# Optimization experiments

Hardware: AMD Instinct MI355X
Metric: run time of the kernel (lower is better)

## Reference

```python
import jax, jax.numpy as jnp
import numpy as np

RADIUS = 0.1
K = 32
NUM_GROUPS = 8
EPS = 1e-5
B, N = 2, 4096
IN_DIM = 13
OUT_DIMS = (64, 64, 128)


def _safe_norm(x, axis=-1, keepdims=False):
    # 2-norm with zero (not NaN) gradient at 0; forward identical to jnp.linalg.norm
    sq = jnp.sum(x * x, axis=axis, keepdims=keepdims)
    nz = sq > 0
    return jnp.where(nz, jnp.sqrt(jnp.where(nz, sq, 1.0)), 0.0)


def _angle(v1, v2):
    y = _safe_norm(jnp.cross(v1, v2), axis=-1)
    x = jnp.sum(v1 * v2, axis=-1)
    deg = (y == 0) & (x == 0)  # degenerate pairs (e.g. self-neighbor): atan2(0,0)=0
    return jnp.where(deg, 0.0, jnp.arctan2(y, jnp.where(deg, 1.0, x)))


def _ball_group(xyz, radius, k):
    # xyz: (B,N,3) -> neighbor indices (B,N,K); pad out-of-radius slots with first valid idx
    b, n, _ = xyz.shape
    sq = jnp.sum((xyz[:, :, None, :] - xyz[:, None, :, :]) ** 2, axis=-1)  # (B,N,N)
    idx = jnp.broadcast_to(jnp.arange(n, dtype=jnp.int32), (b, n, n))
    idx = jnp.where(sq > radius * radius, n, idx)
    idx = jnp.sort(idx, axis=-1)[:, :, :k]  # (B,N,K)
    first = idx[:, :, :1]
    return jnp.where(idx == n, first, idx)


def _group_norm(x, gamma, beta):
    # x: (B,C,K,N), torch GroupNorm(8, C) semantics (biased var, eps=1e-5)
    b, c, k, n = x.shape
    xg = x.reshape(b, NUM_GROUPS, c // NUM_GROUPS, k, n)
    m = jnp.mean(xg, axis=(2, 3, 4), keepdims=True)
    v = jnp.var(xg, axis=(2, 3, 4), keepdims=True)
    xn = ((xg - m) * jax.lax.rsqrt(v + EPS)).reshape(b, c, k, n)
    return xn * gamma[None, :, None, None] + beta[None, :, None, None]


def _forward(feature, xyz, conv0_w, gn0_g, gn0_b, conv1_w, gn1_g, gn1_b,
             conv2_w, gn2_g, gn2_b, wa, wb, wc):
    b = xyz.shape[0]
    idx = _ball_group(xyz, RADIUS, K)                     # (B,N,K) int32
    bidx = jnp.arange(b)[:, None, None]
    grouped_xyz = xyz[bidx, idx]                          # (B,N,K,3)
    grouped_xyz1 = grouped_xyz - xyz[:, :, None, :]       # relative coords
    dists = _safe_norm(grouped_xyz1, axis=-1, keepdims=True)
    grouped_n = feature[bidx, idx]                        # grouped normals (B,N,K,3)
    new_points = jnp.concatenate([grouped_xyz1, dists, grouped_n], axis=-1)  # (B,N,K,7)

    nr = feature[:, :, None, :]                           # (B,N,1,3)
    ppf = jnp.stack([_angle(nr, grouped_xyz1),
                     _angle(grouped_n, grouped_xyz1),
                     _angle(nr, grouped_n)], axis=-1)     # (B,N,K,3)

    xyz6 = jnp.concatenate([jnp.broadcast_to(xyz[:, :, None, :], grouped_xyz.shape),
                            grouped_xyz], axis=-1)        # (B,N,K,6)
    fused = jnp.concatenate([wa * xyz6, wb * new_points[..., :4], wc * ppf], axis=-1)  # (B,N,K,13)

    x = jnp.transpose(fused, (0, 3, 2, 1))                # (B,13,K,N)
    layers = [(conv0_w, gn0_g, gn0_b), (conv1_w, gn1_g, gn1_b), (conv2_w, gn2_g, gn2_b)]
    for i, (w, g, bb) in enumerate(layers):
        x = jnp.einsum('oc,bckn->bokn', w, x)             # 1x1 conv, no bias
        x = _group_norm(x, g, bb)
        if i != len(layers) - 1:
            x = jax.nn.relu(x)
    out = jnp.max(jax.nn.relu(x), axis=2)                 # (B,128,N)
    x = jnp.max(x, axis=2)                                # (B,128,N)
    return (out, x)


def setup_inputs() -> dict:
    key = jax.random.key(0)
    ks = jax.random.split(key, 8)
    xyz = jax.random.uniform(ks[0], (B, N, 3), dtype=jnp.float32)
    feature = jax.random.normal(ks[1], (B, N, 3), dtype=jnp.float32)
    feature = feature / _safe_norm(feature, axis=-1, keepdims=True)  # unit normals
    inp = {'feature': feature, 'xyz': xyz}
    dims = [IN_DIM] + list(OUT_DIMS)
    for i in range(3):
        scale = 1.0 / np.sqrt(dims[i])
        inp[f'conv{i}_w'] = (jax.random.normal(ks[2 + i], (dims[i + 1], dims[i]), dtype=jnp.float32) * scale)
        inp[f'gn{i}_g'] = jnp.ones((dims[i + 1],), jnp.float32)
        inp[f'gn{i}_b'] = jnp.zeros((dims[i + 1],), jnp.float32)
    inp['wa'] = jnp.ones((1,), jnp.float32)
    inp['wb'] = jnp.ones((1,), jnp.float32)
    inp['wc'] = jnp.ones((1,), jnp.float32)
    return inp


def reference(feature, xyz, conv0_w, gn0_g, gn0_b, conv1_w, gn1_g, gn1_b,
              conv2_w, gn2_g, gn2_b, wa, wb, wc):
    return _forward(feature, xyz, conv0_w, gn0_g, gn0_b, conv1_w, gn1_g, gn1_b,
                    conv2_w, gn2_g, gn2_b, wa, wb, wc)
```

## Files before the change

kernel.cpp:

```cpp
#include <hip/hip_runtime.h>
#include <hip/hip_bf16.h>

#define DEVINL __device__ __forceinline__

typedef short short8 __attribute__((ext_vector_type(8)));
typedef float f32x4 __attribute__((ext_vector_type(4)));

namespace {
constexpr int NB = 2;
constexpr int NN = 4096;
constexpr int KK = 32;
constexpr int NP = NN * KK;
constexpr float R2 = 0.01f;
constexpr float GEPS = 1e-5f;
}

DEVINL ushort2 splitbf(float v) {
    unsigned int b = __float_as_uint(v);
    unsigned int hb = b & 0xffff0000u;
    float r = v - __uint_as_float(hb);
    unsigned int lb = __float_as_uint(r);
    ushort2 res;
    res.x = (unsigned short)(hb >> 16);
    res.y = (unsigned short)(lb >> 16);
    return res;
}

DEVINL float angle3(float ax, float ay, float az, float bx, float by, float bz) {
    float crx = ay * bz - az * by;
    float cry = az * bx - ax * bz;
    float crz = ax * by - ay * bx;
    float sq = crx * crx + cry * cry + crz * crz;
    float yv = sq > 0.f ? sqrtf(sq) : 0.f;
    float xv = ax * bx + ay * by + az * bz;
    if (yv == 0.f && xv == 0.f) return 0.f;
    return atan2f(yv, xv);
}

template <int NV>
DEVINL float blockReducePart(float* vals) {
    #pragma unroll
    for (int m = 1; m < 64; m <<= 1) {
        #pragma unroll
        for (int q = 0; q < NV; ++q) vals[q] += __shfl_xor(vals[q], m, 64);
    }
    __shared__ float red[4][NV];
    int lane = threadIdx.x & 63, w = threadIdx.x >> 6;
    if (lane == 0) {
        #pragma unroll
        for (int q = 0; q < NV; ++q) red[w][q] = vals[q];
    }
    __syncthreads();
    float v = 0.f;
    if ((int)threadIdx.x < NV)
        v = red[0][threadIdx.x] + red[1][threadIdx.x] +
            red[2][threadIdx.x] + red[3][threadIdx.x];
    return v;
}

__global__ __launch_bounds__(256) void k_red(const float* __restrict__ part,
                                             float* __restrict__ stats, int nblk) {
    int o = blockIdx.x;
    const float* p = part + (size_t)o * nblk;
    float s = 0.f;
    for (int i = threadIdx.x; i < nblk; i += 256) s += p[i];
    #pragma unroll
    for (int m = 1; m < 64; m <<= 1) s += __shfl_xor(s, m, 64);
    __shared__ float r[4];
    if ((threadIdx.x & 63) == 0) r[threadIdx.x >> 6] = s;
    __syncthreads();
    if (threadIdx.x == 0) stats[o] = r[0] + r[1] + r[2] + r[3];
}

__global__ void k_prep(const float* __restrict__ w0, const float* __restrict__ w1,
                       const float* __restrict__ w2, float* __restrict__ w0t,
                       short* __restrict__ a1hi, short* __restrict__ a1lo,
                       short* __restrict__ a2hi, short* __restrict__ a2lo) {
    int t = threadIdx.x;
    for (int x = t; x < 64 * 13; x += 256) { int o = x / 13, c = x % 13; w0t[c * 64 + o] = w0[x]; }
    for (int x = t; x < 512; x += 256) {
        int lane = x & 63, ks = (x >> 6) & 1, mt = x >> 7;
        int o = mt * 16 + (lane & 15);
        int cb = ks * 32 + (lane >> 4) * 8;
        #pragma unroll
        for (int e = 0; e < 8; ++e) {
            ushort2 s = splitbf(w1[o * 64 + cb + e]);
            a1hi[x * 8 + e] = (short)s.x;
            a1lo[x * 8 + e] = (short)s.y;
        }
    }
    for (int x = t; x < 1024; x += 256) {
        int lane = x & 63, ks = (x >> 6) & 1, mt = x >> 7;
        int o = mt * 16 + (lane & 15);
        int cb = ks * 32 + (lane >> 4) * 8;
        #pragma unroll
        for (int e = 0; e < 8; ++e) {
            ushort2 s = splitbf(w2[o * 64 + cb + e]);
            a2hi[x * 8 + e] = (short)s.x;
            a2lo[x * 8 + e] = (short)s.y;
        }
    }
}

__global__ __launch_bounds__(256) void k_ball(const float* __restrict__ xyz,
                                              int* __restrict__ idx) {
    int wid = blockIdx.x * 4 + (threadIdx.x >> 6);
    int lane = threadIdx.x & 63;
    int b = wid >> 12;
    int i = wid & (NN - 1);
    const float* xb = xyz + b * NN * 3;
    float cx = xb[i * 3 + 0], cy = xb[i * 3 + 1], cz = xb[i * 3 + 2];
    int* out = idx + wid * KK;
    int cnt = 0;
    int firstj = 0;
    for (int base = 0; base < NN; base += 64) {
        int j = base + lane;
        float dx = xb[j * 3 + 0] - cx;
        float dy = xb[j * 3 + 1] - cy;
        float dz = xb[j * 3 + 2] - cz;
        float d2 = __fadd_rn(__fadd_rn(__fmul_rn(dx, dx), __fmul_rn(dy, dy)), __fmul_rn(dz, dz));
        bool valid = d2 <= R2;
        unsigned long long m = __ballot(valid);
        if (cnt == 0 && m != 0ull) firstj = base + (int)__builtin_ctzll(m);
        int pos = (int)__popcll(m & ((1ull << lane) - 1ull));
        if (valid && (cnt + pos) < KK) out[cnt + pos] = j;
        cnt += (int)__popcll(m);
        if (cnt >= KK) break;
    }
    if (cnt < KK) {
        int kpad = cnt + lane;
        if (kpad < KK) out[kpad] = firstj;
    }
}

__global__ __launch_bounds__(256) void k_feat(
    const float* __restrict__ xyz, const float* __restrict__ feat,
    const int* __restrict__ idx, const float* __restrict__ w0t,
    const float* __restrict__ wap, const float* __restrict__ wbp,
    const float* __restrict__ wcp, float* __restrict__ f13,
    float* __restrict__ part0) {
    int t = blockIdx.x * 256 + threadIdx.x;
    int b = t / NP, r = t % NP;
    int i = r >> 5;
    int j = idx[t];
    const float* xb = xyz + b * NN * 3;
    const float* fb = feat + b * NN * 3;
    float cx = xb[i * 3], cy = xb[i * 3 + 1], cz = xb[i * 3 + 2];
    float nx = fb[i * 3], ny = fb[i * 3 + 1], nz = fb[i * 3 + 2];
    float gx = xb[j * 3], gy = xb[j * 3 + 1], gz = xb[j * 3 + 2];
    float mx = fb[j * 3], my = fb[j * 3 + 1], mz = fb[j * 3 + 2];
    float dx = gx - cx, dy = gy - cy, dz = gz - cz;
    float d2 = dx * dx + dy * dy + dz * dz;
    float dist = d2 > 0.f ? sqrtf(d2) : 0.f;
    float a1 = angle3(nx, ny, nz, dx, dy, dz);
    float a2 = angle3(mx, my, mz, dx, dy, dz);
    float a3 = angle3(nx, ny, nz, mx, my, mz);
    float WA = wap[0], WB = wbp[0], WC = wcp[0];
    float f[13] = {WA * cx, WA * cy, WA * cz, WA * gx, WA * gy, WA * gz,
                   WB * dx, WB * dy, WB * dz, WB * dist, WC * a1, WC * a2, WC * a3};
    float* fo = f13 + (size_t)b * 13 * NP + r;
    #pragma unroll
    for (int c = 0; c < 13; ++c) fo[(size_t)c * NP] = f[c];
    float acc[64];
    #pragma unroll
    for (int o = 0; o < 64; ++o) acc[o] = 0.f;
    #pragma unroll
    for (int c = 0; c < 13; ++c) {
        float v = f[c];
        const float* wr = w0t + c * 64;
        #pragma unroll
        for (int o = 0; o < 64; ++o) acc[o] = fmaf(wr[o], v, acc[o]);
    }
    float vals[16];
    #pragma unroll
    for (int g = 0; g < 8; ++g) {
        float sv = 0.f, sq = 0.f;
        #pragma unroll
        for (int c2 = 0; c2 < 8; ++c2) { float v = acc[g * 8 + c2]; sv += v; sq = fmaf(v, v, sq); }
        vals[g * 2] = sv; vals[g * 2 + 1] = sq;
    }
    float pv = blockReducePart<16>(vals);
    if ((int)threadIdx.x < 16) {
        int blkInB = blockIdx.x & 511;
        part0[(size_t)(b * 16 + threadIdx.x) * 512 + blkInB] = pv;
    }
}

__global__ __launch_bounds__(256) void k_conv01m(
    const float* __restrict__ f13, const float* __restrict__ stats0,
    const float* __restrict__ g0, const float* __restrict__ b0,
    const float* __restrict__ w0t,
    const short* __restrict__ a1hi, const short* __restrict__ a1lo,
    float* __restrict__ y1, float* __restrict__ part1) {
    __shared__ __align__(16) short Xhi[128 * 64];
    __shared__ __align__(16) short Xlo[128 * 64];
    __shared__ float Aff[128];
    int t = threadIdx.x, blk = blockIdx.x;
    int b = blk >> 10;
    int blkInB = blk & 1023;
    int pbase = blkInB << 7;
    if (t < 64) {
        int c = t, g = c >> 3;
        const float inv = 1.f / 1048576.f;
        float s = stats0[b * 16 + g * 2], q = stats0[b * 16 + g * 2 + 1];
        float mean = s * inv;
        float var = q * inv - mean * mean;
        float rstd = rsqrtf(var + GEPS);
        float a = rstd * g0[c];
        Aff[c] = a; Aff[64 + c] = fmaf(-mean, a, b0[c]);
    }
    __syncthreads();
    {
        int p = t & 127, chalf = t >> 7;
        const float* fi = f13 + (size_t)b * 13 * NP + pbase + p;
        float fv[13];
        #pragma unroll
        for (int c = 0; c < 13; ++c) fv[c] = fi[(size_t)c * NP];
        float acc[32];
        #pragma unroll
        for (int o = 0; o < 32; ++o) acc[o] = 0.f;
        #pragma unroll
        for (int c = 0; c < 13; ++c) {
            const float* wr = w0t + c * 64 + chalf * 32;
            #pragma unroll
            for (int o = 0; o < 32; ++o) acc[o] = fmaf(wr[o], fv[c], acc[o]);
        }
        int swz = (p & 7) << 4;
        #pragma unroll
        for (int jc = 0; jc < 4; ++jc) {
            int hw[4], lw[4];
            #pragma unroll
            for (int u = 0; u < 4; ++u) {
                int o0 = jc * 8 + u * 2;
                int ch0 = chalf * 32 + o0;
                float v0 = fmaxf(fmaf(Aff[ch0], acc[o0], Aff[64 + ch0]), 0.f);
                float v1 = fmaxf(fmaf(Aff[ch0 + 1], acc[o0 + 1], Aff[64 + ch0 + 1]), 0.f);
                ushort2 s0 = splitbf(v0), s1 = splitbf(v1);
                hw[u] = (int)((unsigned)s0.x | ((unsigned)s1.x << 16));
                lw[u] = (int)((unsigned)s0.y | ((unsigned)s1.y << 16));
            }
            int off = p * 128 + ((chalf * 64 + jc * 16) ^ swz);
            *reinterpret_cast<int4*>((char*)Xhi + off) = make_int4(hw[0], hw[1], hw[2], hw[3]);
            *reinterpret_cast<int4*>((char*)Xlo + off) = make_int4(lw[0], lw[1], lw[2], lw[3]);
        }
    }
    __syncthreads();
    {
        int w = t >> 6, lane = t & 63, col = lane & 15, kb = lane >> 4;
        short8 whi[2], wlo[2];
        #pragma unroll
        for (int ks = 0; ks < 2; ++ks) {
            int fi_ = ((w * 2 + ks) * 64 + lane) * 8;
            whi[ks] = *reinterpret_cast<const short8*>(a1hi + fi_);
            wlo[ks] = *reinterpret_cast<const short8*>(a1lo + fi_);
        }
        float sv = 0.f, sq = 0.f;
        int swzr = (col & 7) << 4;
        float* yb = y1 + (size_t)b * 64 * NP + pbase + col;
        #pragma unroll 2
        for (int s = 0; s < 8; ++s) {
            int rowoff = (s * 16 + col) * 128;
            f32x4 d = {0.f, 0.f, 0.f, 0.f};
            #pragma unroll
            for (int ks = 0; ks < 2; ++ks) {
                int boff = rowoff + ((ks * 64 + kb * 16) ^ swzr);
                short8 bh = *reinterpret_cast<const short8*>((char*)Xhi + boff);
                short8 bl = *reinterpret_cast<const short8*>((char*)Xlo + boff);
                d = __builtin_amdgcn_mfma_f32_16x16x32_bf16(whi[ks], bh, d, 0, 0, 0);
                d = __builtin_amdgcn_mfma_f32_16x16x32_bf16(whi[ks], bl, d, 0, 0, 0);
                d = __builtin_amdgcn_mfma_f32_16x16x32_bf16(wlo[ks], bh, d, 0, 0, 0);
            }
            #pragma unroll
            for (int q = 0; q < 4; ++q) {
                int ch = w * 16 + kb * 4 + q;
                yb[(size_t)ch * NP + s * 16] = d[q];
                sv += d[q];
                sq = fmaf(d[q], d[q], sq);
            }
        }
        #pragma unroll
        for (int m = 1; m <= 16; m <<= 1) {
            sv += __shfl_xor(sv, m, 64);
            sq += __shfl_xor(sq, m, 64);
        }
        if ((lane & 31) == 0) {
            int grp = w * 2 + (lane >> 5);
            size_t o = (size_t)(b * 16 + grp * 2) * 1024 + blkInB;
            part1[o] = sv;
            part1[o + 1024] = sq;
        }
    }
}

__global__ __launch_bounds__(256) void k_conv2m(
    const float* __restrict__ y1, const float* __restrict__ stats1,
    const float* __restrict__ g1, const float* __restrict__ b1,
    const float* __restrict__ g2,
    const short* __restrict__ a2hi, const short* __restrict__ a2lo,
    float* __restrict__ ext, float* __restrict__ part2) {
    __shared__ __align__(16) short Xhi[128 * 64];
    __shared__ __align__(16) short Xlo[128 * 64];
    __shared__ float Aff[128];
    int t = threadIdx.x, blk = blockIdx.x;
    int b = blk >> 10;
    int blkInB = blk & 1023;
    int pbase = blkInB << 7;
    if (t < 64) {
        int c = t, g = c >> 3;
        const float inv = 1.f / 1048576.f;
        float s = stats1[b * 16 + g * 2], q = stats1[b * 16 + g * 2 + 1];
        float mean = s * inv;
        float var = q * inv - mean * mean;
        float rstd = rsqrtf(var + GEPS);
        float a = rstd * g1[c];
        Aff[c] = a; Aff[64 + c] = fmaf(-mean, a, b1[c]);
    }
    __syncthreads();
    {
        int p = t & 127, cblk = t >> 7;
        const float* yi = y1 + (size_t)b * 64 * NP + pbase + p;
        int swz = (p & 7) << 4;
        #pragma unroll
        for (int jc = 0; jc < 4; ++jc) {
            int hw[4], lw[4];
            #pragma unroll
            for (int u = 0; u < 4; ++u) {
                int ch0 = cblk * 32 + jc * 8 + u * 2;
                float v0 = yi[(size_t)ch0 * NP];
                float v1 = yi[(size_t)(ch0 + 1) * NP];
                v0 = fmaxf(fmaf(Aff[ch0], v0, Aff[64 + ch0]), 0.f);
                v1 = fmaxf(fmaf(Aff[ch0 + 1], v1, Aff[64 + ch0 + 1]), 0.f);
                ushort2 s0 = splitbf(v0), s1 = splitbf(v1);
                hw[u] = (int)((unsigned)s0.x | ((unsigned)s1.x << 16));
                lw[u] = (int)((unsigned)s0.y | ((unsigned)s1.y << 16));
            }
            int off = p * 128 + ((cblk * 64 + jc * 16) ^ swz);
            *reinterpret_cast<int4*>((char*)Xhi + off) = make_int4(hw[0], hw[1], hw[2], hw[3]);
            *reinterpret_cast<int4*>((char*)Xlo + off) = make_int4(lw[0], lw[1], lw[2], lw[3]);
        }
    }
    __syncthreads();
    {
        int w = t >> 6, lane = t & 63, col = lane & 15, kb = lane >> 4;
        int mt0 = w * 2;
        short8 whi[2][2], wlo[2][2];
        #pragma unroll
        for (int m = 0; m < 2; ++m)
            #pragma unroll
            for (int ks = 0; ks < 2; ++ks) {
                int fi_ = (((mt0 + m) * 2 + ks) * 64 + lane) * 8;
                whi[m][ks] = *reinterpret_cast<const short8*>(a2hi + fi_);
                wlo[m][ks] = *reinterpret_cast<const short8*>(a2lo + fi_);
            }
        float gv[2][4];
        #pragma unroll
        for (int m = 0; m < 2; ++m)
            #pragma unroll
            for (int q = 0; q < 4; ++q) gv[m][q] = g2[(mt0 + m) * 16 + kb * 4 + q];
        float sv[2] = {0.f, 0.f}, sq[2] = {0.f, 0.f};
        int swzr = (col & 7) << 4;
        int ibase = pbase >> 5;
        #pragma unroll
        for (int sp = 0; sp < 4; ++sp) {
            f32x4 dp0[2], dp1[2];
            #pragma unroll
            for (int ss = 0; ss < 2; ++ss) {
                int rowoff = ((sp * 2 + ss) * 16 + col) * 128;
                short8 bh[2], bl[2];
                #pragma unroll
                for (int ks = 0; ks < 2; ++ks) {
                    int boff = rowoff + ((ks * 64 + kb * 16) ^ swzr);
                    bh[ks] = *reinterpret_cast<const short8*>((char*)Xhi + boff);
                    bl[ks] = *reinterpret_cast<const short8*>((char*)Xlo + boff);
                }
                #pragma unroll
                for (int m = 0; m < 2; ++m) {
                    f32x4 d = {0.f, 0.f, 0.f, 0.f};
                    #pragma unroll
                    for (int ks = 0; ks < 2; ++ks) {
                        d = __builtin_amdgcn_mfma_f32_16x16x32_bf16(whi[m][ks], bh[ks], d, 0, 0, 0);
                        d = __builtin_amdgcn_mfma_f32_16x16x32_bf16(whi[m][ks], bl[ks], d, 0, 0, 0);
                        d = __builtin_amdgcn_mfma_f32_16x16x32_bf16(wlo[m][ks], bh[ks], d, 0, 0, 0);
                    }
                    #pragma unroll
                    for (int q = 0; q < 4; ++q) {
                        sv[m] += d[q];
                        sq[m] = fmaf(d[q], d[q], sq[m]);
                    }
                    if (ss == 0) dp0[m] = d; else dp1[m] = d;
                }
            }
            #pragma unroll
            for (int m = 0; m < 2; ++m) {
                float e[4];
                #pragma unroll
                for (int q = 0; q < 4; ++q) {
                    bool mx = gv[m][q] >= 0.f;
                    e[q] = mx ? fmaxf(dp0[m][q], dp1[m][q]) : fminf(dp0[m][q], dp1[m][q]);
                    #pragma unroll
                    for (int sh = 1; sh <= 8; sh <<= 1) {
                        float o = __shfl_xor(e[q], sh, 64);
                        e[q] = mx ? fmaxf(e[q], o) : fminf(e[q], o);
                    }
                }
                if (col == 0) {
                    #pragma unroll
                    for (int q = 0; q < 4; ++q) {
                        int ch = (mt0 + m) * 16 + kb * 4 + q;
                        ext[((size_t)b * 128 + ch) * NN + ibase + sp] = e[q];
                    }
                }
            }
        }
        #pragma unroll
        for (int m = 0; m < 2; ++m) {
            #pragma unroll
            for (int sh = 1; sh <= 32; sh <<= 1) {
                sv[m] += __shfl_xor(sv[m], sh, 64);
                sq[m] += __shfl_xor(sq[m], sh, 64);
            }
        }
        if (lane == 0) {
            #pragma unroll
            for (int m = 0; m < 2; ++m) {
                size_t o = (size_t)(b * 16 + (mt0 + m) * 2) * 1024 + blkInB;
                part2[o] = sv[m];
                part2[o + 1024] = sq[m];
            }
        }
    }
}

__global__ __launch_bounds__(256) void k_final(
    const float* __restrict__ ext, const float* __restrict__ stats2,
    const float* __restrict__ g2, const float* __restrict__ b2,
    float* __restrict__ outp) {
    __shared__ float A[128], Bc[128];
    int t = blockIdx.x * 256 + threadIdx.x;
    int b = t / (128 * NN);
    int rem = t - b * 128 * NN;
    int c = rem >> 12;
    if (threadIdx.x < 128) {
        int cc = threadIdx.x, g = cc >> 4;
        const float inv = 1.f / 2097152.f;
        float s = stats2[b * 16 + g * 2], q = stats2[b * 16 + g * 2 + 1];
        float mean = s * inv;
        float var = q * inv - mean * mean;
        float rstd = rsqrtf(var + GEPS);
        float a = rstd * g2[cc];
        A[cc] = a; Bc[cc] = fmaf(-mean, a, b2[cc]);
    }
    __syncthreads();
    float v = ext[t];
    float val = fmaf(A[c], v, Bc[c]);
    outp[t] = fmaxf(val, 0.f);
    outp[NB * 128 * NN + t] = val;
}

extern "C" void kernel_launch(void* const* d_in, const int* in_sizes, int n_in,
                              void* d_out, int out_size, void* d_ws, size_t ws_size,
                              hipStream_t stream) {
    const float* feat = (const float*)d_in[0];
    const float* xyz  = (const float*)d_in[1];
    const float* w0 = (const float*)d_in[2];
    const float* g0 = (const float*)d_in[3];
    const float* b0 = (const float*)d_in[4];
    const float* w1 = (const float*)d_in[5];
    const float* g1 = (const float*)d_in[6];
    const float* b1 = (const float*)d_in[7];
    const float* w2 = (const float*)d_in[8];
    const float* g2 = (const float*)d_in[9];
    const float* b2 = (const float*)d_in[10];
    const float* wa = (const float*)d_in[11];
    const float* wb = (const float*)d_in[12];
    const float* wc = (const float*)d_in[13];

    char* ws = (char*)d_ws;
    float* stats = (float*)ws;
    float* w0t  = (float*)(ws + 4096);
    short* a1hi = (short*)(ws + 16384);
    short* a1lo = (short*)(ws + 24576);
    short* a2hi = (short*)(ws + 32768);
    short* a2lo = (short*)(ws + 49152);
    int*   idx  = (int*)(ws + 65536);
    float* part0 = (float*)(ws + 1179648);
    float* part1 = (float*)(ws + 1245184);
    float* part2 = (float*)(ws + 1376256);
    float* f13  = (float*)(ws + (2ull << 20));
    float* y1   = (float*)(ws + (16ull << 20));
    float* ext  = (float*)(ws + (80ull << 20));

    hipLaunchKernelGGL(k_prep, dim3(1), dim3(256), 0, stream,
                       w0, w1, w2, w0t, a1hi, a1lo, a2hi, a2lo);
    hipLaunchKernelGGL(k_ball, dim3((NB * NN) / 4), dim3(256), 0, stream, xyz, idx);
    hipLaunchKernelGGL(k_feat, dim3((NB * NP) / 256), dim3(256), 0, stream,
                       xyz, feat, idx, w0t, wa, wb, wc, f13, part0);
    hipLaunchKernelGGL(k_red, dim3(32), dim3(256), 0, stream, part0, stats, 512);
    hipLaunchKernelGGL(k_conv01m, dim3((NB * NP) / 128), dim3(256), 0, stream,
                       f13, stats, g0, b0, w0t, a1hi, a1lo, y1, part1);
    hipLaunchKernelGGL(k_red, dim3(32), dim3(256), 0, stream, part1, stats + 32, 1024);
    hipLaunchKernelGGL(k_conv2m, dim3((NB * NP) / 128), dim3(256), 0, stream,
                       y1, stats + 32, g1, b1, g2, a2hi, a2lo, ext, part2);
    hipLaunchKernelGGL(k_red, dim3(32), dim3(256), 0, stream, part2, stats + 64, 1024);
    hipLaunchKernelGGL(k_final, dim3((NB * 128 * NN) / 256), dim3(256), 0, stream,
                       ext, stats + 64, g2, b2, (float*)d_out);
}
```

Before: 214.9 us.

## Recompute conv0/conv1 inside conv2 kernel instead of storing y1 intermediate

The first conv1 pass now only computes group-norm statistics and no longer writes the 64-channel y1 tensor. The conv2 kernel recomputes conv0, its norm and ReLU, and the conv1 MFMA from f13. It then applies the second norm and ReLU in registers and restages the result in shared memory for conv2. This removes a large global write and read of y1, at the cost of recomputing conv0/conv1, reading f13 twice, and higher register pressure and extra barriers in the fused kernel.

```diff
diff --git a/kernel.cpp b/kernel.cpp
--- a/kernel.cpp
+++ b/kernel.cpp
@@ -186,12 +186,12 @@
     }
 }
 
-__global__ __launch_bounds__(256) void k_conv01m(
+__global__ __launch_bounds__(256) void k_stats01(
     const float* __restrict__ f13, const float* __restrict__ stats0,
     const float* __restrict__ g0, const float* __restrict__ b0,
     const float* __restrict__ w0t,
     const short* __restrict__ a1hi, const short* __restrict__ a1lo,
-    float* __restrict__ y1, float* __restrict__ part1) {
+    float* __restrict__ part1) {
     __shared__ __align__(16) short Xhi[128 * 64];
     __shared__ __align__(16) short Xlo[128 * 64];
     __shared__ float Aff[128];
@@ -256,7 +256,6 @@
         }
         float sv = 0.f, sq = 0.f;
         int swzr = (col & 7) << 4;
-        float* yb = y1 + (size_t)b * 64 * NP + pbase + col;
         #pragma unroll 2
         for (int s = 0; s < 8; ++s) {
             int rowoff = (s * 16 + col) * 128;
@@ -272,8 +271,6 @@
             }
             #pragma unroll
             for (int q = 0; q < 4; ++q) {
-                int ch = w * 16 + kb * 4 + q;
-                yb[(size_t)ch * NP + s * 16] = d[q];
                 sv += d[q];
                 sq = fmaf(d[q], d[q], sq);
             }
@@ -292,15 +289,19 @@
     }
 }
 
-__global__ __launch_bounds__(256) void k_conv2m(
-    const float* __restrict__ y1, const float* __restrict__ stats1,
+__global__ __launch_bounds__(256) void k_fused2(
+    const float* __restrict__ f13, const float* __restrict__ stats0,
+    const float* __restrict__ g0, const float* __restrict__ b0,
+    const float* __restrict__ w0t,
+    const short* __restrict__ a1hi, const short* __restrict__ a1lo,
+    const float* __restrict__ stats1,
     const float* __restrict__ g1, const float* __restrict__ b1,
     const float* __restrict__ g2,
     const short* __restrict__ a2hi, const short* __restrict__ a2lo,
     float* __restrict__ ext, float* __restrict__ part2) {
     __shared__ __align__(16) short Xhi[128 * 64];
     __shared__ __align__(16) short Xlo[128 * 64];
-    __shared__ float Aff[128];
+    __shared__ float Aff[256];
     int t = threadIdx.x, blk = blockIdx.x;
     int b = blk >> 10;
     int blkInB = blk & 1023;
@@ -308,40 +309,110 @@
     if (t < 64) {
         int c = t, g = c >> 3;
         const float inv = 1.f / 1048576.f;
-        float s = stats1[b * 16 + g * 2], q = stats1[b * 16 + g * 2 + 1];
+        float s = stats0[b * 16 + g * 2], q = stats0[b * 16 + g * 2 + 1];
         float mean = s * inv;
         float var = q * inv - mean * mean;
         float rstd = rsqrtf(var + GEPS);
-        float a = rstd * g1[c];
-        Aff[c] = a; Aff[64 + c] = fmaf(-mean, a, b1[c]);
+        float a = rstd * g0[c];
+        Aff[c] = a; Aff[64 + c] = fmaf(-mean, a, b0[c]);
+        float s1 = stats1[b * 16 + g * 2], q1 = stats1[b * 16 + g * 2 + 1];
+        float mean1 = s1 * inv;
+        float var1 = q1 * inv - mean1 * mean1;
+        float rstd1 = rsqrtf(var1 + GEPS);
+        float a1 = rstd1 * g1[c];
+        Aff[128 + c] = a1; Aff[192 + c] = fmaf(-mean1, a1, b1[c]);
     }
     __syncthreads();
     {
-        int p = t & 127, cblk = t >> 7;
-        const float* yi = y1 + (size_t)b * 64 * NP + pbase + p;
+        int p = t & 127, chalf = t >> 7;
+        const float* fi = f13 + (size_t)b * 13 * NP + pbase + p;
+        float fv[13];
+        #pragma unroll
+        for (int c = 0; c < 13; ++c) fv[c] = fi[(size_t)c * NP];
+        float acc[32];
+        #pragma unroll
+        for (int o = 0; o < 32; ++o) acc[o] = 0.f;
+        #pragma unroll
+        for (int c = 0; c < 13; ++c) {
+            const float* wr = w0t + c * 64 + chalf * 32;
+            #pragma unroll
+            for (int o = 0; o < 32; ++o) acc[o] = fmaf(wr[o], fv[c], acc[o]);
+        }
         int swz = (p & 7) << 4;
         #pragma unroll
         for (int jc = 0; jc < 4; ++jc) {
             int hw[4], lw[4];
             #pragma unroll
             for (int u = 0; u < 4; ++u) {
-                int ch0 = cblk * 32 + jc * 8 + u * 2;
-                float v0 = yi[(size_t)ch0 * NP];
-                float v1 = yi[(size_t)(ch0 + 1) * NP];
-                v0 = fmaxf(fmaf(Aff[ch0], v0, Aff[64 + ch0]), 0.f);
-                v1 = fmaxf(fmaf(Aff[ch0 + 1], v1, Aff[64 + ch0 + 1]), 0.f);
+                int o0 = jc * 8 + u * 2;
+                int ch0 = chalf * 32 + o0;
+                float v0 = fmaxf(fmaf(Aff[ch0], acc[o0], Aff[64 + ch0]), 0.f);
+                float v1 = fmaxf(fmaf(Aff[ch0 + 1], acc[o0 + 1], Aff[64 + ch0 + 1]), 0.f);
                 ushort2 s0 = splitbf(v0), s1 = splitbf(v1);
                 hw[u] = (int)((unsigned)s0.x | ((unsigned)s1.x << 16));
                 lw[u] = (int)((unsigned)s0.y | ((unsigned)s1.y << 16));
             }
-            int off = p * 128 + ((cblk * 64 + jc * 16) ^ swz);
+            int off = p * 128 + ((chalf * 64 + jc * 16) ^ swz);
             *reinterpret_cast<int4*>((char*)Xhi + off) = make_int4(hw[0], hw[1], hw[2], hw[3]);
             *reinterpret_cast<int4*>((char*)Xlo + off) = make_int4(lw[0], lw[1], lw[2], lw[3]);
         }
     }
     __syncthreads();
+    int w = t >> 6, lane = t & 63, col = lane & 15, kb = lane >> 4;
+    int swzr = (col & 7) << 4;
+    float y[8][4];
     {
-        int w = t >> 6, lane = t & 63, col = lane & 15, kb = lane >> 4;
+        short8 whi[2], wlo[2];
+        #pragma unroll
+        for (int ks = 0; ks < 2; ++ks) {
+            int fi_ = ((w * 2 + ks) * 64 + lane) * 8;
+            whi[ks] = *reinterpret_cast<const short8*>(a1hi + fi_);
+            wlo[ks] = *reinterpret_cast<const short8*>(a1lo + fi_);
+        }
+        #pragma unroll 2
+        for (int s = 0; s < 8; ++s) {
+            int rowoff = (s * 16 + col) * 128;
+            f32x4 d = {0.f, 0.f, 0.f, 0.f};
+            #pragma unroll
+            for (int ks = 0; ks < 2; ++ks) {
+                int boff = rowoff + ((ks * 64 + kb * 16) ^ swzr);
+                short8 bh = *reinterpret_cast<const short8*>((char*)Xhi + boff);
+                short8 bl = *reinterpret_cast<const short8*>((char*)Xlo + boff);
+                d = __builtin_amdgcn_mfma_f32_16x16x32_bf16(whi[ks], bh, d, 0, 0, 0);
+                d = __builtin_amdgcn_mfma_f32_16x16x32_bf16(whi[ks], bl, d, 0, 0, 0);
+                d = __builtin_amdgcn_mfma_f32_16x16x32_bf16(wlo[ks], bh, d, 0, 0, 0);
+            }
+            #pragma unroll
+            for (int q = 0; q < 4; ++q) y[s][q] = d[q];
+        }
+    }
+    __syncthreads();
+    {
+        float a1v[4], b1v[4];
+        #pragma unroll
+        for (int q = 0; q < 4; ++q) {
+            int c = w * 16 + kb * 4 + q;
+            a1v[q] = Aff[128 + c]; b1v[q] = Aff[192 + c];
+        }
+        #pragma unroll
+        for (int s = 0; s < 8; ++s) {
+            int hw[2], lw[2];
+            #pragma unroll
+            for (int u = 0; u < 2; ++u) {
+                float v0 = fmaxf(fmaf(a1v[u * 2], y[s][u * 2], b1v[u * 2]), 0.f);
+                float v1 = fmaxf(fmaf(a1v[u * 2 + 1], y[s][u * 2 + 1], b1v[u * 2 + 1]), 0.f);
+                ushort2 s0 = splitbf(v0), s1 = splitbf(v1);
+                hw[u] = (int)((unsigned)s0.x | ((unsigned)s1.x << 16));
+                lw[u] = (int)((unsigned)s0.y | ((unsigned)s1.y << 16));
+            }
+            int p = s * 16 + col;
+            int off = p * 128 + ((w * 32 + kb * 8) ^ swzr);
+            *reinterpret_cast<int2*>((char*)Xhi + off) = make_int2(hw[0], hw[1]);
+            *reinterpret_cast<int2*>((char*)Xlo + off) = make_int2(lw[0], lw[1]);
+        }
+    }
+    __syncthreads();
+    {
         int mt0 = w * 2;
         short8 whi[2][2], wlo[2][2];
         #pragma unroll
@@ -358,7 +429,6 @@
             #pragma unroll
             for (int q = 0; q < 4; ++q) gv[m][q] = g2[(mt0 + m) * 16 + kb * 4 + q];
         float sv[2] = {0.f, 0.f}, sq[2] = {0.f, 0.f};
-        int swzr = (col & 7) << 4;
         int ibase = pbase >> 5;
         #pragma unroll
         for (int sp = 0; sp < 4; ++sp) {
@@ -487,8 +557,7 @@
     float* part1 = (float*)(ws + 1245184);
     float* part2 = (float*)(ws + 1376256);
     float* f13  = (float*)(ws + (2ull << 20));
-    float* y1   = (float*)(ws + (16ull << 20));
-    float* ext  = (float*)(ws + (80ull << 20));
+    float* ext  = (float*)(ws + (16ull << 20));
 
     hipLaunchKernelGGL(k_prep, dim3(1), dim3(256), 0, stream,
                        w0, w1, w2, w0t, a1hi, a1lo, a2hi, a2lo);
@@ -496,11 +565,12 @@
     hipLaunchKernelGGL(k_feat, dim3((NB * NP) / 256), dim3(256), 0, stream,
                        xyz, feat, idx, w0t, wa, wb, wc, f13, part0);
     hipLaunchKernelGGL(k_red, dim3(32), dim3(256), 0, stream, part0, stats, 512);
-    hipLaunchKernelGGL(k_conv01m, dim3((NB * NP) / 128), dim3(256), 0, stream,
-                       f13, stats, g0, b0, w0t, a1hi, a1lo, y1, part1);
+    hipLaunchKernelGGL(k_stats01, dim3((NB * NP) / 128), dim3(256), 0, stream,
+                       f13, stats, g0, b0, w0t, a1hi, a1lo, part1);
     hipLaunchKernelGGL(k_red, dim3(32), dim3(256), 0, stream, part1, stats + 32, 1024);
-    hipLaunchKernelGGL(k_conv2m, dim3((NB * NP) / 128), dim3(256), 0, stream,
-                       y1, stats + 32, g1, b1, g2, a2hi, a2lo, ext, part2);
+    hipLaunchKernelGGL(k_fused2, dim3((NB * NP) / 128), dim3(256), 0, stream,
+                       f13, stats, g0, b0, w0t, a1hi, a1lo,
+                       stats + 32, g1, b1, g2, a2hi, a2lo, ext, part2);
     hipLaunchKernelGGL(k_red, dim3(32), dim3(256), 0, stream, part2, stats + 64, 1024);
     hipLaunchKernelGGL(k_final, dim3((NB * 128 * NN) / 256), dim3(256), 0, stream,
                        ext, stats + 64, g2, b2, (float*)d_out);
```

Result: no change. 217.8 us (+1.3%).
